# Kernel tuning notes

Measured on AMD Instinct MI355X. Metric: run time of the kernel, lower is better.

## Reference

```python
import jax, jax.numpy as jnp
import numpy as np

# GCN over dependency trees (aryehgigi/gcn-over-pruned-trees), eval mode:
# dropout = identity, rnn=False, dep_dim=0, no_adj=False.
# Per layer l: Ax = adj @ x ; AxW = Linear_l(Ax) + Linear_l(x) (bias counted twice,
# faithful to `self.W[l](Ax) + self.W[l](gcn_inputs)`) ; AxW /= (adj.sum(2)+1) ; relu.

B, L = 128, 256
VOCAB, EMB, POSV, POSD, NERV, NERD, MEM = 50000, 300, 52, 30, 20, 30, 200
IN_DIM = EMB + POSD + NERD  # 360


def setup_inputs() -> dict:
    key = jax.random.key(0)
    ks = jax.random.split(key, 11)
    words = jax.random.randint(ks[0], (B, L), 0, VOCAB)
    pos = jax.random.randint(ks[1], (B, L), 0, POSV)
    ner = jax.random.randint(ks[2], (B, L), 0, NERV)
    adj = (jax.random.uniform(ks[3], (B, L, L)) < 0.05).astype(jnp.float32)
    emb_W = jax.random.normal(ks[4], (VOCAB, EMB), jnp.float32) * 0.1
    pos_W = jax.random.normal(ks[5], (POSV, POSD), jnp.float32) * 0.1
    ner_W = jax.random.normal(ks[6], (NERV, NERD), jnp.float32) * 0.1
    W0 = jax.random.normal(ks[7], (MEM, IN_DIM), jnp.float32) * (1.0 / np.sqrt(IN_DIM))
    b0 = jnp.zeros((MEM,), jnp.float32)
    W1 = jax.random.normal(ks[8], (MEM, MEM), jnp.float32) * (1.0 / np.sqrt(MEM))
    b1 = jnp.zeros((MEM,), jnp.float32)
    return {"words": words, "pos": pos, "ner": ner, "adj": adj,
            "emb_W": emb_W, "pos_W": pos_W, "ner_W": ner_W,
            "W0": W0, "b0": b0, "W1": W1, "b1": b1}


def reference(words, pos, ner, adj, emb_W, pos_W, ner_W, W0, b0, W1, b1):
    # embedding lookups + concat -> [B, L, IN_DIM]
    x = jnp.concatenate([emb_W[words], pos_W[pos], ner_W[ner]], axis=2)
    denom = jnp.sum(adj, axis=2, keepdims=True) + 1.0  # [B, L, 1]
    mask = ((jnp.sum(adj, axis=2) + jnp.sum(adj, axis=1)) == 0)[..., None]  # [B, L, 1]
    for W, b in ((W0, b0), (W1, b1)):
        Ax = jnp.einsum('bij,bjd->bid', adj, x)  # message passing
        # W(Ax) + W(x) == (Ax + x) @ W.T + 2*b  (bias applied twice, as in source)
        h = (jnp.einsum('bld,md->blm', Ax + x, W) + 2.0 * b) / denom
        x = jax.nn.relu(h)
    return (x, mask)
```

## Files before the change

kernel.cpp:

```cpp
#include <hip/hip_runtime.h>
#include <hip/hip_bf16.h>
#include <stdint.h>

typedef __attribute__((ext_vector_type(8))) short short8;
typedef __attribute__((ext_vector_type(4))) float f32x4;

#define NB 128
#define NL 256
#define NROWS 32768
#define IN_DIM 360
#define KP1 384
#define MEM 200
#define NP 256
#define OUT_X (NROWS * MEM)
#define YTP 264
#define BUFSZ 20480
#define YTOFF 40960


__device__ __forceinline__ unsigned short f2b(float f) {
    unsigned u = __builtin_bit_cast(unsigned, f);
    unsigned r = (u + 0x7FFFu + ((u >> 16) & 1u)) >> 16;
    return (unsigned short)r;
}

__device__ __forceinline__ short8 gather_chunk(int chunk, const float* __restrict__ er,
                                               const float* __restrict__ pr,
                                               const float* __restrict__ nr) {
    float v[8];
    if (chunk < 37) {
        const float* s = er + chunk * 8;
        float4 a = *(const float4*)s;
        float4 b = *(const float4*)(s + 4);
        v[0] = a.x; v[1] = a.y; v[2] = a.z; v[3] = a.w;
        v[4] = b.x; v[5] = b.y; v[6] = b.z; v[7] = b.w;
    } else if (chunk == 37) {
        float4 a = *(const float4*)(er + 296);
        v[0] = a.x; v[1] = a.y; v[2] = a.z; v[3] = a.w;
        v[4] = 0.f; v[5] = 0.f; v[6] = 0.f; v[7] = 0.f;
    } else if (chunk <= 41) {
        int k0 = chunk * 8 - 304;
        #pragma unroll
        for (int i = 0; i < 8; ++i) v[i] = (k0 + i < 30) ? pr[k0 + i] : 0.f;
    } else if (chunk <= 45) {
        int k0 = chunk * 8 - 336;
        #pragma unroll
        for (int i = 0; i < 8; ++i) v[i] = (k0 + i < 30) ? nr[k0 + i] : 0.f;
    } else {
        #pragma unroll
        for (int i = 0; i < 8; ++i) v[i] = 0.f;
    }
    short8 r;
    #pragma unroll
    for (int i = 0; i < 8; ++i) r[i] = (short)f2b(v[i]);
    return r;
}

__global__ void prep_weights(const float* __restrict__ W0, const float* __restrict__ W1,
                             short* __restrict__ W0p, short* __restrict__ W1p,
                             unsigned* __restrict__ colnz) {
    int idx = blockIdx.x * 256 + threadIdx.x;
    if (idx < NROWS) colnz[idx] = 0u;
    if (idx < NP * KP1) {
        int n = idx / KP1, kp = idx - n * KP1;
        float v = 0.f;
        if (n < MEM) {
            if (kp < 300)                   v = W0[n * IN_DIM + kp];
            else if (kp >= 304 && kp < 334) v = W0[n * IN_DIM + 300 + (kp - 304)];
            else if (kp >= 336 && kp < 366) v = W0[n * IN_DIM + 330 + (kp - 336)];
        }
        W0p[idx] = (short)f2b(v);
    } else {
        int i2 = idx - NP * KP1;
        if (i2 < NP * NP) {
            int n = i2 >> 8, k = i2 & 255;
            float v = (n < MEM && k < MEM) ? W1[n * MEM + k] : 0.f;
            W1p[i2] = (short)f2b(v);
        }
    }
}

__global__ void adjrow_kernel(const float* __restrict__ adj, float* __restrict__ dinv,
                              float* __restrict__ rsum, unsigned short* __restrict__ Sbf,
                              unsigned* __restrict__ colnz) {
    int row = blockIdx.x * 4 + (threadIdx.x >> 6);
    int lane = threadIdx.x & 63;
    const float4* ar = (const float4*)(adj + (size_t)row * NL);
    float4 v = ar[lane];
    float s = v.x + v.y + v.z + v.w;
    #pragma unroll
    for (int off = 32; off >= 1; off >>= 1) s += __shfl_xor(s, off);
    int rloc = row & 255;
    float d0 = v.x + ((lane * 4 + 0) == rloc ? 1.f : 0.f);
    float d1 = v.y + ((lane * 4 + 1) == rloc ? 1.f : 0.f);
    float d2 = v.z + ((lane * 4 + 2) == rloc ? 1.f : 0.f);
    float d3 = v.w + ((lane * 4 + 3) == rloc ? 1.f : 0.f);
    ushort4 st; st.x = f2b(d0); st.y = f2b(d1); st.z = f2b(d2); st.w = f2b(d3);
    *(ushort4*)(Sbf + (size_t)row * NL + lane * 4) = st;
    if (lane == 0) { rsum[row] = s; dinv[row] = 1.0f / (s + 1.0f); }
    unsigned* cz = colnz + ((row >> 8) << 8);
    if (v.x != 0.f) atomicOr(&cz[lane * 4 + 0], 1u);
    if (v.y != 0.f) atomicOr(&cz[lane * 4 + 1], 1u);
    if (v.z != 0.f) atomicOr(&cz[lane * 4 + 2], 1u);
    if (v.w != 0.f) atomicOr(&cz[lane * 4 + 3], 1u);
}

__global__ void mask_kernel(const float* __restrict__ rsum, const unsigned* __restrict__ colnz,
                            float* __restrict__ outm) {
    int r = blockIdx.x * 256 + threadIdx.x;
    outm[r] = (rsum[r] == 0.f && colnz[r] == 0u) ? 1.0f : 0.0f;
}

template <int FINAL>
__global__ __launch_bounds__(512, 4) void fused_kernel(
    const short* __restrict__ A, int lda, int nkt,
    const short* __restrict__ Bp, int ldb,
    const unsigned short* __restrict__ Sbf,
    const float* __restrict__ dinv, const float* __restrict__ bias,
    const int* __restrict__ words, const int* __restrict__ pos, const int* __restrict__ ner,
    const float* __restrict__ embW, const float* __restrict__ posW,
    const float* __restrict__ nerW,
    short* __restrict__ x1b, float* __restrict__ outx) {
    extern __shared__ char smem[];
    unsigned short* Yt = (unsigned short*)(smem + YTOFF);

    int bi = blockIdx.x;
    int batch = bi & 127, sl = bi >> 7;

    int tid = threadIdx.x;
    int lane = tid & 63, wid = tid >> 6;
    int wr = wid >> 1, wc = wid & 1;
    int lr = lane & 15, lc = lane >> 4;

    const short* Bb = Bp + (size_t)sl * 64 * ldb;
    const short* Sb = (const short*)(Sbf + (size_t)batch * NL * NL);

    int r0s = tid >> 2, c0s = tid & 3;
    int r1s = r0s + 128;
    int offA0 = r0s * 64 + (c0s ^ ((r0s >> 1) & 3)) * 16;
    int offA1 = r1s * 64 + (c0s ^ ((r1s >> 1) & 3)) * 16;
    const short* Sp0 = Sb + (size_t)r0s * NL + c0s * 8;
    const short* Sp1 = Sb + (size_t)r1s * NL + c0s * 8;
    int offB = 0; const short* Bpp = nullptr;
    if (tid < 256) {
        int br = tid >> 2, bc = tid & 3;
        offB = 16384 + br * 64 + (bc ^ ((br >> 1) & 3)) * 16;
        Bpp = Bb + (size_t)br * ldb + bc * 8;
    }

    const short* Ap0 = nullptr; const short* Ap1 = nullptr;
    const float *er0 = nullptr, *pr0 = nullptr, *nr0 = nullptr;
    const float *er1 = nullptr, *pr1 = nullptr, *nr1 = nullptr;
    if (FINAL == 0) {
        int g0 = batch * NL + r0s, g1 = g0 + 128;
        er0 = embW + (size_t)words[g0] * 300;
        pr0 = posW + (size_t)pos[g0] * 30;
        nr0 = nerW + (size_t)ner[g0] * 30;
        er1 = embW + (size_t)words[g1] * 300;
        pr1 = posW + (size_t)pos[g1] * 30;
        nr1 = nerW + (size_t)ner[g1] * 30;
    } else {
        const short* Ab = A + (size_t)batch * NL * lda;
        Ap0 = Ab + (size_t)r0s * lda + c0s * 8;
        Ap1 = Ab + (size_t)r1s * lda + c0s * 8;
    }
    #define LOADA(kt, o0, o1) do {                                  \
        if (FINAL == 0) {                                           \
            int ch_ = (kt) * 4 + c0s;                               \
            (o0) = gather_chunk(ch_, er0, pr0, nr0);                \
            (o1) = gather_chunk(ch_, er1, pr1, nr1);                \
        } else {                                                    \
            (o0) = *(const short8*)(Ap0 + (kt) * 32);               \
            (o1) = *(const short8*)(Ap1 + (kt) * 32);               \
        }                                                           \
    } while (0)

    f32x4 acc[4][2] = {};
    short8 aR0, aR1, bR;
    LOADA(0, aR0, aR1);
    if (tid < 256) bR = *(const short8*)Bpp;
    *(short8*)(smem + offA0) = aR0;
    *(short8*)(smem + offA1) = aR1;
    if (tid < 256) *(short8*)(smem + offB) = bR;
    LOADA(1, aR0, aR1);
    if (tid < 256) bR = *(const short8*)(Bpp + 32);
    __syncthreads();

    short8 sA0, sA1, sB0, sB1;
    for (int kt = 0; kt < nkt; ++kt) {
        char* base_ = smem + (kt & 1) * BUFSZ;
        short8 af[4], bf[2];
        #pragma unroll
        for (int mi = 0; mi < 4; ++mi) {
            int row = wr * 64 + mi * 16 + lr;
            int cs = lc ^ ((row >> 1) & 3);
            af[mi] = *(const short8*)(base_ + row * 64 + cs * 16);
        }
        #pragma unroll
        for (int ni = 0; ni < 2; ++ni) {
            int row = wc * 32 + ni * 16 + lr;
            int cs = lc ^ ((row >> 1) & 3);
            bf[ni] = *(const short8*)(base_ + 16384 + row * 64 + cs * 16);
        }
        if (kt + 1 < nkt) {
            char* nb_ = smem + ((kt + 1) & 1) * BUFSZ;
            *(short8*)(nb_ + offA0) = aR0;
            *(short8*)(nb_ + offA1) = aR1;
            if (tid < 256) *(short8*)(nb_ + offB) = bR;
        }
        if (kt + 2 < nkt) {
            LOADA(kt + 2, aR0, aR1);
            if (tid < 256) bR = *(const short8*)(Bpp + (kt + 2) * 32);
        } else if (kt + 2 == nkt) {
            sA0 = *(const short8*)Sp0;
            sA1 = *(const short8*)Sp1;
        } else if (kt + 2 == nkt + 1) {
            sB0 = *(const short8*)(Sp0 + 32);
            sB1 = *(const short8*)(Sp1 + 32);
        }
        #pragma unroll
        for (int mi = 0; mi < 4; ++mi)
            #pragma unroll
            for (int ni = 0; ni < 2; ++ni)
                acc[mi][ni] = __builtin_amdgcn_mfma_f32_16x16x32_bf16(af[mi], bf[ni], acc[mi][ni], 0, 0, 0);
        __syncthreads();
    }
    #undef LOADA

    #pragma unroll
    for (int mi = 0; mi < 4; ++mi)
        #pragma unroll
        for (int ni = 0; ni < 2; ++ni) {
            f32x4 v = acc[mi][ni];
            ushort4 st; st.x = f2b(v[0]); st.y = f2b(v[1]); st.z = f2b(v[2]); st.w = f2b(v[3]);
            int col = wc * 32 + ni * 16 + lr;
            int row0 = wr * 64 + mi * 16 + lc * 4;
            *(ushort4*)(Yt + (size_t)col * YTP + row0) = st;
        }
    *(short8*)(smem + offA0) = sA0;
    *(short8*)(smem + offA1) = sA1;
    sA0 = *(const short8*)(Sp0 + 64);
    sA1 = *(const short8*)(Sp1 + 64);
    __syncthreads();

    f32x4 acc2[4][2] = {};
    #pragma unroll
    for (int kt = 0; kt < 8; ++kt) {
        char* base_ = smem + (kt & 1) * BUFSZ;
        short8 ay[4], bs[2];
        #pragma unroll
        for (int mi = 0; mi < 4; ++mi)
            ay[mi] = *(const short8*)(Yt + (size_t)(mi * 16 + lr) * YTP + kt * 32 + lc * 8);
        #pragma unroll
        for (int ni = 0; ni < 2; ++ni) {
            int row = wid * 32 + ni * 16 + lr;
            int cs = lc ^ ((row >> 1) & 3);
            bs[ni] = *(const short8*)(base_ + row * 64 + cs * 16);
        }
        if (kt + 1 < 8) {
            char* nb_ = smem + ((kt + 1) & 1) * BUFSZ;
            if ((kt & 1) == 0) {
                *(short8*)(nb_ + offA0) = sB0;
                *(short8*)(nb_ + offA1) = sB1;
                if (kt + 3 < 8) {
                    sB0 = *(const short8*)(Sp0 + (kt + 3) * 32);
                    sB1 = *(const short8*)(Sp1 + (kt + 3) * 32);
                }
            } else {
                *(short8*)(nb_ + offA0) = sA0;
                *(short8*)(nb_ + offA1) = sA1;
                if (kt + 3 < 8) {
                    sA0 = *(const short8*)(Sp0 + (kt + 3) * 32);
                    sA1 = *(const short8*)(Sp1 + (kt + 3) * 32);
                }
            }
        }
        #pragma unroll
        for (int mi = 0; mi < 4; ++mi)
            #pragma unroll
            for (int ni = 0; ni < 2; ++ni)
                acc2[mi][ni] = __builtin_amdgcn_mfma_f32_16x16x32_bf16(ay[mi], bs[ni], acc2[mi][ni], 0, 0, 0);
        if (kt + 1 < 8) __syncthreads();
    }

    #pragma unroll
    for (int ni = 0; ni < 2; ++ni) {
        int g = batch * NL + wid * 32 + ni * 16 + lr;
        float di = dinv[g];
        #pragma unroll
        for (int mi = 0; mi < 4; ++mi) {
            int col0 = sl * 64 + mi * 16 + lc * 4;
            float4 bv;
            if (col0 < MEM) bv = *(const float4*)(bias + col0);
            else { bv.x = 0.f; bv.y = 0.f; bv.z = 0.f; bv.w = 0.f; }
            f32x4 z = acc2[mi][ni];
            float h0 = fmaxf((z[0] + 2.f * bv.x) * di, 0.f);
            float h1 = fmaxf((z[1] + 2.f * bv.y) * di, 0.f);
            float h2 = fmaxf((z[2] + 2.f * bv.z) * di, 0.f);
            float h3 = fmaxf((z[3] + 2.f * bv.w) * di, 0.f);
            if (FINAL == 0) {
                ushort4 st; st.x = f2b(h0); st.y = f2b(h1); st.z = f2b(h2); st.w = f2b(h3);
                *(ushort4*)((unsigned short*)x1b + (size_t)g * NP + col0) = st;
            } else if (col0 < MEM) {
                float4 o; o.x = h0; o.y = h1; o.z = h2; o.w = h3;
                *(float4*)(outx + (size_t)g * MEM + col0) = o;
            }
        }
    }
}

extern "C" void kernel_launch(void* const* d_in, const int* in_sizes, int n_in,
                              void* d_out, int out_size, void* d_ws, size_t ws_size,
                              hipStream_t stream) {
    const int*   words = (const int*)d_in[0];
    const int*   pos   = (const int*)d_in[1];
    const int*   ner   = (const int*)d_in[2];
    const float* adj   = (const float*)d_in[3];
    const float* embW  = (const float*)d_in[4];
    const float* posW  = (const float*)d_in[5];
    const float* nerW  = (const float*)d_in[6];
    const float* W0    = (const float*)d_in[7];
    const float* b0    = (const float*)d_in[8];
    const float* W1    = (const float*)d_in[9];
    const float* b1    = (const float*)d_in[10];
    float* out = (float*)d_out;

    char* ws = (char*)d_ws;
    size_t off = 0;
    short* W0p = (short*)(ws + off);        off += (size_t)NP * KP1 * 2;
    short* W1p = (short*)(ws + off);        off += (size_t)NP * NP * 2;
    short* X1b = (short*)(ws + off);        off += (size_t)NROWS * NP * 2;
    float* dinv = (float*)(ws + off);       off += (size_t)NROWS * 4;
    float* rsum = (float*)(ws + off);       off += (size_t)NROWS * 4;
    unsigned* colnz = (unsigned*)(ws + off); off += (size_t)NROWS * 4;
    unsigned short* Sbf = (unsigned short*)(ws + off); off += (size_t)NROWS * NL * 2;

    prep_weights<<<(NP * KP1 + NP * NP + 255) / 256, 256, 0, stream>>>(W0, W1, W0p, W1p, colnz);
    adjrow_kernel<<<NROWS / 4, 256, 0, stream>>>(adj, dinv, rsum, Sbf, colnz);
    mask_kernel<<<NROWS / 256, 256, 0, stream>>>(rsum, colnz, out + OUT_X);

    const int ldsB = YTOFF + 64 * YTP * 2;
    fused_kernel<0><<<NB * 4, 512, ldsB, stream>>>(nullptr, KP1, KP1 / 32, W0p, KP1,
                                                   Sbf, dinv, b0,
                                                   words, pos, ner, embW, posW, nerW,
                                                   X1b, nullptr);
    fused_kernel<1><<<NB * 4, 512, ldsB, stream>>>(X1b, NP, NP / 32, W1p, NP,
                                                   Sbf, dinv, b1,
                                                   nullptr, nullptr, nullptr, nullptr, nullptr, nullptr,
                                                   nullptr, out);
}
```

Baseline: 82.79 us.

## Load GEMM B-operands directly from global into registers, fold mask kernel

The weight tiles and the adjacency tiles are no longer staged through LDS. Each wave now loads its MFMA B fragments straight from global memory into registers, prefetched one k-step ahead. This shrinks the LDS buffers, removes the LDS stores and reads for B, and drops the barriers in the second GEMM loop. The separate mask kernel is also folded into the first fused kernel to save a launch. In exchange, each wave does redundant global loads (two wc columns share rows), which lean on L2/L1 bandwidth and latency.

```diff
diff --git a/kernel.cpp b/kernel.cpp
--- a/kernel.cpp
+++ b/kernel.cpp
@@ -14,8 +14,8 @@
 #define NP 256
 #define OUT_X (NROWS * MEM)
 #define YTP 264
-#define BUFSZ 20480
-#define YTOFF 40960
+#define BUFSZ 16384
+#define YTOFF 32768
 
 
 __device__ __forceinline__ unsigned short f2b(float f) {
@@ -105,12 +105,6 @@
     if (v.w != 0.f) atomicOr(&cz[lane * 4 + 3], 1u);
 }
 
-__global__ void mask_kernel(const float* __restrict__ rsum, const unsigned* __restrict__ colnz,
-                            float* __restrict__ outm) {
-    int r = blockIdx.x * 256 + threadIdx.x;
-    outm[r] = (rsum[r] == 0.f && colnz[r] == 0u) ? 1.0f : 0.0f;
-}
-
 template <int FINAL>
 __global__ __launch_bounds__(512, 4) void fused_kernel(
     const short* __restrict__ A, int lda, int nkt,
@@ -120,6 +114,8 @@
     const int* __restrict__ words, const int* __restrict__ pos, const int* __restrict__ ner,
     const float* __restrict__ embW, const float* __restrict__ posW,
     const float* __restrict__ nerW,
+    const float* __restrict__ rsum, const unsigned* __restrict__ colnz,
+    float* __restrict__ maskout,
     short* __restrict__ x1b, float* __restrict__ outx) {
     extern __shared__ char smem[];
     unsigned short* Yt = (unsigned short*)(smem + YTOFF);
@@ -132,21 +128,22 @@
     int wr = wid >> 1, wc = wid & 1;
     int lr = lane & 15, lc = lane >> 4;
 
-    const short* Bb = Bp + (size_t)sl * 64 * ldb;
+    if (FINAL == 0 && sl == 0 && tid < 256) {
+        int r = batch * NL + tid;
+        maskout[r] = (rsum[r] == 0.f && colnz[r] == 0u) ? 1.0f : 0.0f;
+    }
+
     const short* Sb = (const short*)(Sbf + (size_t)batch * NL * NL);
 
     int r0s = tid >> 2, c0s = tid & 3;
     int r1s = r0s + 128;
     int offA0 = r0s * 64 + (c0s ^ ((r0s >> 1) & 3)) * 16;
     int offA1 = r1s * 64 + (c0s ^ ((r1s >> 1) & 3)) * 16;
-    const short* Sp0 = Sb + (size_t)r0s * NL + c0s * 8;
-    const short* Sp1 = Sb + (size_t)r1s * NL + c0s * 8;
-    int offB = 0; const short* Bpp = nullptr;
-    if (tid < 256) {
-        int br = tid >> 2, bc = tid & 3;
-        offB = 16384 + br * 64 + (bc ^ ((br >> 1) & 3)) * 16;
-        Bpp = Bb + (size_t)br * ldb + bc * 8;
-    }
+
+    const short* Bf0 = Bp + (size_t)(sl * 64 + wc * 32 + lr) * ldb + lc * 8;
+    const short* Bf1 = Bf0 + (size_t)16 * ldb;
+    const short* Sw0 = Sb + (size_t)(wid * 32 + lr) * NL + lc * 8;
+    const short* Sw1 = Sw0 + (size_t)16 * NL;
 
     const short* Ap0 = nullptr; const short* Ap1 = nullptr;
     const float *er0 = nullptr, *pr0 = nullptr, *nr0 = nullptr;
@@ -176,56 +173,47 @@
     } while (0)
 
     f32x4 acc[4][2] = {};
-    short8 aR0, aR1, bR;
+    short8 aR0, aR1;
     LOADA(0, aR0, aR1);
-    if (tid < 256) bR = *(const short8*)Bpp;
     *(short8*)(smem + offA0) = aR0;
     *(short8*)(smem + offA1) = aR1;
-    if (tid < 256) *(short8*)(smem + offB) = bR;
     LOADA(1, aR0, aR1);
-    if (tid < 256) bR = *(const short8*)(Bpp + 32);
+    short8 bf0 = *(const short8*)Bf0;
+    short8 bf1 = *(const short8*)Bf1;
     __syncthreads();
 
-    short8 sA0, sA1, sB0, sB1;
     for (int kt = 0; kt < nkt; ++kt) {
         char* base_ = smem + (kt & 1) * BUFSZ;
-        short8 af[4], bf[2];
+        short8 af[4];
         #pragma unroll
         for (int mi = 0; mi < 4; ++mi) {
             int row = wr * 64 + mi * 16 + lr;
             int cs = lc ^ ((row >> 1) & 3);
             af[mi] = *(const short8*)(base_ + row * 64 + cs * 16);
         }
-        #pragma unroll
-        for (int ni = 0; ni < 2; ++ni) {
-            int row = wc * 32 + ni * 16 + lr;
-            int cs = lc ^ ((row >> 1) & 3);
-            bf[ni] = *(const short8*)(base_ + 16384 + row * 64 + cs * 16);
-        }
         if (kt + 1 < nkt) {
             char* nb_ = smem + ((kt + 1) & 1) * BUFSZ;
             *(short8*)(nb_ + offA0) = aR0;
             *(short8*)(nb_ + offA1) = aR1;
-            if (tid < 256) *(short8*)(nb_ + offB) = bR;
-        }
-        if (kt + 2 < nkt) {
-            LOADA(kt + 2, aR0, aR1);
-            if (tid < 256) bR = *(const short8*)(Bpp + (kt + 2) * 32);
-        } else if (kt + 2 == nkt) {
-            sA0 = *(const short8*)Sp0;
-            sA1 = *(const short8*)Sp1;
-        } else if (kt + 2 == nkt + 1) {
-            sB0 = *(const short8*)(Sp0 + 32);
-            sB1 = *(const short8*)(Sp1 + 32);
-        }
-        #pragma unroll
-        for (int mi = 0; mi < 4; ++mi)
-            #pragma unroll
-            for (int ni = 0; ni < 2; ++ni)
-                acc[mi][ni] = __builtin_amdgcn_mfma_f32_16x16x32_bf16(af[mi], bf[ni], acc[mi][ni], 0, 0, 0);
+        }
+        if (kt + 2 < nkt) LOADA(kt + 2, aR0, aR1);
+        short8 bf0n, bf1n;
+        if (kt + 1 < nkt) {
+            bf0n = *(const short8*)(Bf0 + (kt + 1) * 32);
+            bf1n = *(const short8*)(Bf1 + (kt + 1) * 32);
+        }
+        #pragma unroll
+        for (int mi = 0; mi < 4; ++mi) {
+            acc[mi][0] = __builtin_amdgcn_mfma_f32_16x16x32_bf16(af[mi], bf0, acc[mi][0], 0, 0, 0);
+            acc[mi][1] = __builtin_amdgcn_mfma_f32_16x16x32_bf16(af[mi], bf1, acc[mi][1], 0, 0, 0);
+        }
+        if (kt + 1 < nkt) { bf0 = bf0n; bf1 = bf1n; }
         __syncthreads();
     }
     #undef LOADA
+
+    short8 bs0 = *(const short8*)Sw0;
+    short8 bs1 = *(const short8*)Sw1;
 
     #pragma unroll
     for (int mi = 0; mi < 4; ++mi)
@@ -237,50 +225,26 @@
             int row0 = wr * 64 + mi * 16 + lc * 4;
             *(ushort4*)(Yt + (size_t)col * YTP + row0) = st;
         }
-    *(short8*)(smem + offA0) = sA0;
-    *(short8*)(smem + offA1) = sA1;
-    sA0 = *(const short8*)(Sp0 + 64);
-    sA1 = *(const short8*)(Sp1 + 64);
     __syncthreads();
 
     f32x4 acc2[4][2] = {};
     #pragma unroll
     for (int kt = 0; kt < 8; ++kt) {
-        char* base_ = smem + (kt & 1) * BUFSZ;
-        short8 ay[4], bs[2];
+        short8 ay[4];
         #pragma unroll
         for (int mi = 0; mi < 4; ++mi)
             ay[mi] = *(const short8*)(Yt + (size_t)(mi * 16 + lr) * YTP + kt * 32 + lc * 8);
-        #pragma unroll
-        for (int ni = 0; ni < 2; ++ni) {
-            int row = wid * 32 + ni * 16 + lr;
-            int cs = lc ^ ((row >> 1) & 3);
-            bs[ni] = *(const short8*)(base_ + row * 64 + cs * 16);
-        }
+        short8 bs0n, bs1n;
         if (kt + 1 < 8) {
-            char* nb_ = smem + ((kt + 1) & 1) * BUFSZ;
-            if ((kt & 1) == 0) {
-                *(short8*)(nb_ + offA0) = sB0;
-                *(short8*)(nb_ + offA1) = sB1;
-                if (kt + 3 < 8) {
-                    sB0 = *(const short8*)(Sp0 + (kt + 3) * 32);
-                    sB1 = *(const short8*)(Sp1 + (kt + 3) * 32);
-                }
-            } else {
-                *(short8*)(nb_ + offA0) = sA0;
-                *(short8*)(nb_ + offA1) = sA1;
-                if (kt + 3 < 8) {
-                    sA0 = *(const short8*)(Sp0 + (kt + 3) * 32);
-                    sA1 = *(const short8*)(Sp1 + (kt + 3) * 32);
-                }
-            }
-        }
-        #pragma unroll
-        for (int mi = 0; mi < 4; ++mi)
-            #pragma unroll
-            for (int ni = 0; ni < 2; ++ni)
-                acc2[mi][ni] = __builtin_amdgcn_mfma_f32_16x16x32_bf16(ay[mi], bs[ni], acc2[mi][ni], 0, 0, 0);
-        if (kt + 1 < 8) __syncthreads();
+            bs0n = *(const short8*)(Sw0 + (kt + 1) * 32);
+            bs1n = *(const short8*)(Sw1 + (kt + 1) * 32);
+        }
+        #pragma unroll
+        for (int mi = 0; mi < 4; ++mi) {
+            acc2[mi][0] = __builtin_amdgcn_mfma_f32_16x16x32_bf16(ay[mi], bs0, acc2[mi][0], 0, 0, 0);
+            acc2[mi][1] = __builtin_amdgcn_mfma_f32_16x16x32_bf16(ay[mi], bs1, acc2[mi][1], 0, 0, 0);
+        }
+        if (kt + 1 < 8) { bs0 = bs0n; bs1 = bs1n; }
     }
 
     #pragma unroll
@@ -337,15 +301,16 @@
 
     prep_weights<<<(NP * KP1 + NP * NP + 255) / 256, 256, 0, stream>>>(W0, W1, W0p, W1p, colnz);
     adjrow_kernel<<<NROWS / 4, 256, 0, stream>>>(adj, dinv, rsum, Sbf, colnz);
-    mask_kernel<<<NROWS / 256, 256, 0, stream>>>(rsum, colnz, out + OUT_X);
 
     const int ldsB = YTOFF + 64 * YTP * 2;
     fused_kernel<0><<<NB * 4, 512, ldsB, stream>>>(nullptr, KP1, KP1 / 32, W0p, KP1,
                                                    Sbf, dinv, b0,
                                                    words, pos, ner, embW, posW, nerW,
+                                                   rsum, colnz, out + OUT_X,
                                                    X1b, nullptr);
     fused_kernel<1><<<NB * 4, 512, ldsB, stream>>>(X1b, NP, NP / 32, W1p, NP,
                                                    Sbf, dinv, b1,
                                                    nullptr, nullptr, nullptr, nullptr, nullptr, nullptr,
+                                                   nullptr, nullptr, nullptr,
                                                    nullptr, out);
 }
```

Result: slower. 94.75 us (+14.5%).

## Deepen global prefetch to four stages and fold mask kernel into fused kernel

Applied to the files above, without the earlier changes.

The mask computation moves from its own kernel launch into the first fused kernel, where the first column slice of each batch writes it, removing one launch. The first GEMM's main loop is restructured as a manually unrolled 4-step macro with four register buffers. Global loads are issued four k-tiles ahead instead of two, hiding more latency. The extra live short8 registers raise register pressure under launch_bounds(512,4), which could cause spills. The loop also assumes nkt is a multiple of 4 (12 and 8 hold).

```diff
diff --git a/kernel.cpp b/kernel.cpp
--- a/kernel.cpp
+++ b/kernel.cpp
@@ -105,12 +105,6 @@
     if (v.w != 0.f) atomicOr(&cz[lane * 4 + 3], 1u);
 }
 
-__global__ void mask_kernel(const float* __restrict__ rsum, const unsigned* __restrict__ colnz,
-                            float* __restrict__ outm) {
-    int r = blockIdx.x * 256 + threadIdx.x;
-    outm[r] = (rsum[r] == 0.f && colnz[r] == 0u) ? 1.0f : 0.0f;
-}
-
 template <int FINAL>
 __global__ __launch_bounds__(512, 4) void fused_kernel(
     const short* __restrict__ A, int lda, int nkt,
@@ -120,6 +114,8 @@
     const int* __restrict__ words, const int* __restrict__ pos, const int* __restrict__ ner,
     const float* __restrict__ embW, const float* __restrict__ posW,
     const float* __restrict__ nerW,
+    const float* __restrict__ rsum, const unsigned* __restrict__ colnz,
+    float* __restrict__ maskout,
     short* __restrict__ x1b, float* __restrict__ outx) {
     extern __shared__ char smem[];
     unsigned short* Yt = (unsigned short*)(smem + YTOFF);
@@ -131,6 +127,11 @@
     int lane = tid & 63, wid = tid >> 6;
     int wr = wid >> 1, wc = wid & 1;
     int lr = lane & 15, lc = lane >> 4;
+
+    if (FINAL == 0 && sl == 0 && tid < 256) {
+        int r = batch * NL + tid;
+        maskout[r] = (rsum[r] == 0.f && colnz[r] == 0u) ? 1.0f : 0.0f;
+    }
 
     const short* Bb = Bp + (size_t)sl * 64 * ldb;
     const short* Sb = (const short*)(Sbf + (size_t)batch * NL * NL);
@@ -176,55 +177,71 @@
     } while (0)
 
     f32x4 acc[4][2] = {};
-    short8 aR0, aR1, bR;
-    LOADA(0, aR0, aR1);
-    if (tid < 256) bR = *(const short8*)Bpp;
-    *(short8*)(smem + offA0) = aR0;
-    *(short8*)(smem + offA1) = aR1;
-    if (tid < 256) *(short8*)(smem + offB) = bR;
-    LOADA(1, aR0, aR1);
-    if (tid < 256) bR = *(const short8*)(Bpp + 32);
+    short8 sA0, sA1, sB0, sB1;
+
+    short8 a0_0, a0_1, a1_0, a1_1, a2_0, a2_1, a3_0, a3_1;
+    short8 bb0, bb1, bb2, bb3;
+    LOADA(0, a0_0, a0_1);
+    if (tid < 256) bb0 = *(const short8*)Bpp;
+    *(short8*)(smem + offA0) = a0_0;
+    *(short8*)(smem + offA1) = a0_1;
+    if (tid < 256) *(short8*)(smem + offB) = bb0;
+    LOADA(1, a1_0, a1_1);
+    LOADA(2, a2_0, a2_1);
+    LOADA(3, a3_0, a3_1);
+    if (tid < 256) {
+        bb1 = *(const short8*)(Bpp + 32);
+        bb2 = *(const short8*)(Bpp + 64);
+        bb3 = *(const short8*)(Bpp + 96);
+    }
     __syncthreads();
 
-    short8 sA0, sA1, sB0, sB1;
-    for (int kt = 0; kt < nkt; ++kt) {
-        char* base_ = smem + (kt & 1) * BUFSZ;
-        short8 af[4], bf[2];
-        #pragma unroll
-        for (int mi = 0; mi < 4; ++mi) {
-            int row = wr * 64 + mi * 16 + lr;
-            int cs = lc ^ ((row >> 1) & 3);
-            af[mi] = *(const short8*)(base_ + row * 64 + cs * 16);
-        }
-        #pragma unroll
-        for (int ni = 0; ni < 2; ++ni) {
-            int row = wc * 32 + ni * 16 + lr;
-            int cs = lc ^ ((row >> 1) & 3);
-            bf[ni] = *(const short8*)(base_ + 16384 + row * 64 + cs * 16);
-        }
-        if (kt + 1 < nkt) {
-            char* nb_ = smem + ((kt + 1) & 1) * BUFSZ;
-            *(short8*)(nb_ + offA0) = aR0;
-            *(short8*)(nb_ + offA1) = aR1;
-            if (tid < 256) *(short8*)(nb_ + offB) = bR;
-        }
-        if (kt + 2 < nkt) {
-            LOADA(kt + 2, aR0, aR1);
-            if (tid < 256) bR = *(const short8*)(Bpp + (kt + 2) * 32);
-        } else if (kt + 2 == nkt) {
-            sA0 = *(const short8*)Sp0;
-            sA1 = *(const short8*)Sp1;
-        } else if (kt + 2 == nkt + 1) {
-            sB0 = *(const short8*)(Sp0 + 32);
-            sB1 = *(const short8*)(Sp1 + 32);
-        }
-        #pragma unroll
-        for (int mi = 0; mi < 4; ++mi)
-            #pragma unroll
-            for (int ni = 0; ni < 2; ++ni)
-                acc[mi][ni] = __builtin_amdgcn_mfma_f32_16x16x32_bf16(af[mi], bf[ni], acc[mi][ni], 0, 0, 0);
-        __syncthreads();
-    }
+    #define STEP(kt, P, WA0, WA1, WB, LA0, LA1, LB) do {                        \
+        char* base_ = smem + (P) * BUFSZ;                                       \
+        short8 af[4], bf[2];                                                    \
+        _Pragma("unroll")                                                       \
+        for (int mi = 0; mi < 4; ++mi) {                                        \
+            int row = wr * 64 + mi * 16 + lr;                                   \
+            int cs = lc ^ ((row >> 1) & 3);                                     \
+            af[mi] = *(const short8*)(base_ + row * 64 + cs * 16);              \
+        }                                                                       \
+        _Pragma("unroll")                                                       \
+        for (int ni = 0; ni < 2; ++ni) {                                        \
+            int row = wc * 32 + ni * 16 + lr;                                   \
+            int cs = lc ^ ((row >> 1) & 3);                                     \
+            bf[ni] = *(const short8*)(base_ + 16384 + row * 64 + cs * 16);      \
+        }                                                                       \
+        if ((kt) + 1 < nkt) {                                                   \
+            char* nb_ = smem + (1 - (P)) * BUFSZ;                               \
+            *(short8*)(nb_ + offA0) = WA0;                                      \
+            *(short8*)(nb_ + offA1) = WA1;                                      \
+            if (tid < 256) *(short8*)(nb_ + offB) = WB;                         \
+        }                                                                       \
+        if ((kt) + 4 < nkt) {                                                   \
+            LOADA((kt) + 4, LA0, LA1);                                          \
+            if (tid < 256) LB = *(const short8*)(Bpp + ((kt) + 4) * 32);        \
+        } else if ((kt) + 4 == nkt) {                                           \
+            sA0 = *(const short8*)Sp0;                                          \
+            sA1 = *(const short8*)Sp1;                                          \
+        } else if ((kt) + 4 == nkt + 1) {                                       \
+            sB0 = *(const short8*)(Sp0 + 32);                                   \
+            sB1 = *(const short8*)(Sp1 + 32);                                   \
+        }                                                                       \
+        _Pragma("unroll")                                                       \
+        for (int mi = 0; mi < 4; ++mi) {                                        \
+            acc[mi][0] = __builtin_amdgcn_mfma_f32_16x16x32_bf16(af[mi], bf[0], acc[mi][0], 0, 0, 0); \
+            acc[mi][1] = __builtin_amdgcn_mfma_f32_16x16x32_bf16(af[mi], bf[1], acc[mi][1], 0, 0, 0); \
+        }                                                                       \
+        __syncthreads();                                                        \
+    } while (0)
+
+    for (int kb = 0; kb < nkt; kb += 4) {
+        STEP(kb + 0, 0, a1_0, a1_1, bb1, a0_0, a0_1, bb0);
+        STEP(kb + 1, 1, a2_0, a2_1, bb2, a1_0, a1_1, bb1);
+        STEP(kb + 2, 0, a3_0, a3_1, bb3, a2_0, a2_1, bb2);
+        STEP(kb + 3, 1, a0_0, a0_1, bb0, a3_0, a3_1, bb3);
+    }
+    #undef STEP
     #undef LOADA
 
     #pragma unroll
@@ -276,10 +293,10 @@
             }
         }
         #pragma unroll
-        for (int mi = 0; mi < 4; ++mi)
-            #pragma unroll
-            for (int ni = 0; ni < 2; ++ni)
-                acc2[mi][ni] = __builtin_amdgcn_mfma_f32_16x16x32_bf16(ay[mi], bs[ni], acc2[mi][ni], 0, 0, 0);
+        for (int mi = 0; mi < 4; ++mi) {
+            acc2[mi][0] = __builtin_amdgcn_mfma_f32_16x16x32_bf16(ay[mi], bs[0], acc2[mi][0], 0, 0, 0);
+            acc2[mi][1] = __builtin_amdgcn_mfma_f32_16x16x32_bf16(ay[mi], bs[1], acc2[mi][1], 0, 0, 0);
+        }
         if (kt + 1 < 8) __syncthreads();
     }
 
@@ -337,15 +354,16 @@
 
     prep_weights<<<(NP * KP1 + NP * NP + 255) / 256, 256, 0, stream>>>(W0, W1, W0p, W1p, colnz);
     adjrow_kernel<<<NROWS / 4, 256, 0, stream>>>(adj, dinv, rsum, Sbf, colnz);
-    mask_kernel<<<NROWS / 256, 256, 0, stream>>>(rsum, colnz, out + OUT_X);
 
     const int ldsB = YTOFF + 64 * YTP * 2;
     fused_kernel<0><<<NB * 4, 512, ldsB, stream>>>(nullptr, KP1, KP1 / 32, W0p, KP1,
                                                    Sbf, dinv, b0,
                                                    words, pos, ner, embW, posW, nerW,
+                                                   rsum, colnz, out + OUT_X,
                                                    X1b, nullptr);
     fused_kernel<1><<<NB * 4, 512, ldsB, stream>>>(X1b, NP, NP / 32, W1p, NP,
                                                    Sbf, dinv, b1,
                                                    nullptr, nullptr, nullptr, nullptr, nullptr, nullptr,
+                                                   nullptr, nullptr, nullptr,
                                                    nullptr, out);
 }
```

Measured after the change: 107.8 us. 1.3x slower.
